# Optimization experiments

Hardware: AMD Instinct MI355X
Metric: run time of the kernel (lower is better)

Reference implementation:

```python
import jax, jax.numpy as jnp
import numpy as np

B, LQ, LK, C = 16, 1024, 1024, 512
WH = int(LQ ** 0.5)  # 32


def setup_inputs() -> dict:
    key = jax.random.key(0)
    ks = jax.random.split(key, 6)
    s1 = 1.0 / np.sqrt(LK)
    return {
        "query": jax.random.normal(ks[0], (B, LQ, C), jnp.float32),
        "key": jax.random.normal(ks[1], (B, LK, C), jnp.float32),
        "value": jax.random.normal(ks[2], (B, LK, C), jnp.float32),
        # nn.Linear weights, stored [out_features, in_features] like torch
        "w1": jax.random.normal(ks[3], (LK, LK), jnp.float32) * s1,
        "w2": jax.random.normal(ks[4], (LK, LK), jnp.float32) * s1,
        "w3": jax.random.normal(ks[5], (1, LK), jnp.float32) * s1,
    }


def reference(query, key, value, w1, w2, w3):
    # cosine-similarity matrix (computed under no_grad in the original)
    q = query / 100.0
    k = key / 100.0
    qn = jnp.sqrt(jnp.sum(q * q, axis=-1))[:, :, None]   # [B, LQ, 1]
    kn = jnp.sqrt(jnp.sum(k * k, axis=-1))[:, None, :]   # [B, 1, LK]
    outer = qn * kn                                       # rank-1 outer product [B, LQ, LK]
    upper = jnp.einsum('bqc,bkc->bqk', q, k)              # [B, LQ, LK]
    similar_rev = jax.lax.stop_gradient(upper / (outer + 1e-6))

    # 3-layer MLP gating over the LK axis -> scalar weight per query row
    h = jax.nn.gelu(jnp.einsum('bqk,ok->bqo', similar_rev, w1), approximate=False)
    h = jax.nn.gelu(jnp.einsum('bqk,ok->bqo', h, w2), approximate=False)
    w = jnp.einsum('bqk,ok->bqo', h, w3)[..., 0]          # [B, LQ]

    # weight^T @ similar_rev / wh, then tanh -> per-key scalar gate [B, LK, 1]
    weight = jnp.einsum('bq,bqk->bk', w, similar_rev) / WH
    weight = jnp.tanh(weight)[:, :, None]

    # value modulation + residual
    return value * weight + value
```

## Files before the change

### kernel.cpp

```cpp
#include <hip/hip_runtime.h>
#include <hip/hip_bf16.h>

#define B_  16
#define LQ_ 1024
#define LK_ 1024
#define C_  512

typedef __attribute__((ext_vector_type(4))) float f32x4;
typedef __attribute__((ext_vector_type(8))) short bf16x8;

__device__ __forceinline__ float bf2f(ushort u) {
  union { unsigned int i; float f; } v; v.i = ((unsigned int)u) << 16; return v.f;
}
__device__ __forceinline__ ushort f2bf(float f) {
  union { float f; unsigned int i; } v; v.f = f;
  unsigned int r = v.i + 0x7fffu + ((v.i >> 16) & 1u);
  return (ushort)(r >> 16);
}
__device__ __forceinline__ float gelu_exact(float x) {
  return 0.5f * x * (1.0f + erff(x * 0.70710678118654752f));
}

__device__ __forceinline__ void gload_lds16(const ushort* g, ushort* l) {
  __builtin_amdgcn_global_load_lds(
      (const __attribute__((address_space(1))) void*)g,
      (__attribute__((address_space(3))) void*)l, 16, 0, 0);
}

__global__ __launch_bounds__(256) void prep_qk(const float* __restrict__ x,
                                               ushort* __restrict__ xb,
                                               float* __restrict__ norms) {
  int wid = blockIdx.x * 4 + (threadIdx.x >> 6);
  int lane = threadIdx.x & 63;
  const float* xr = x + (long)wid * C_;
  ushort* xo = xb + (long)wid * C_;
  float ss = 0.f;
#pragma unroll
  for (int i0 = 0; i0 < 2; ++i0) {
    int i = lane * 4 + i0 * 256;
    float4 v = *(const float4*)(xr + i);
    ss += v.x * v.x + v.y * v.y + v.z * v.z + v.w * v.w;
    ushort4 o;
    o.x = f2bf(v.x); o.y = f2bf(v.y); o.z = f2bf(v.z); o.w = f2bf(v.w);
    *(ushort4*)(xo + i) = o;
  }
#pragma unroll
  for (int off = 32; off > 0; off >>= 1) ss += __shfl_xor(ss, off);
  if (lane == 0) norms[wid] = sqrtf(ss);
}

__global__ __launch_bounds__(256) void conv_bf16(const float* __restrict__ x,
                                                 ushort* __restrict__ o, int n4) {
  int i = blockIdx.x * 256 + threadIdx.x;
  if (i < n4) {
    float4 v = *(const float4*)(x + (long)i * 4);
    ushort4 u;
    u.x = f2bf(v.x); u.y = f2bf(v.y); u.z = f2bf(v.z); u.w = f2bf(v.w);
    *(ushort4*)(o + (long)i * 4) = u;
  }
}

#define BK 32

template <int EPI>
__global__ __launch_bounds__(256, 2) void gemm_nt(
    const ushort* __restrict__ A, const ushort* __restrict__ Bm,
    ushort* __restrict__ Cc, int K, long sA, long sB, long sC,
    const float* __restrict__ qn, const float* __restrict__ kn) {
  int b = blockIdx.z;
  A += (long)b * sA;
  Bm += (long)b * sB;
  Cc += (long)b * sC;
  const int bm = blockIdx.y * 128, bn = blockIdx.x * 128;

  __shared__ ushort At[128][32];
  __shared__ ushort Bt[128][32];

  int tid = threadIdx.x;
  int lane = tid & 63, w = tid >> 6;
  int wr = w >> 1, wc = w & 1;
  int l16 = lane & 15, lhi = lane >> 4;

  f32x4 acc[4][4] = {};

  int c0 = tid, c1 = tid + 256;
  int r0 = c0 >> 2, cb0 = (c0 & 3) ^ ((r0 >> 1) & 3);
  int r1 = c1 >> 2, cb1 = (c1 & 3) ^ ((r1 >> 1) & 3);
  int wbase0 = (tid & ~63);
  int wbase1 = wbase0 + 256;

  const ushort* Ar0 = A + (long)(bm + r0) * K + cb0 * 8;
  const ushort* Ar1 = A + (long)(bm + r1) * K + cb1 * 8;
  const ushort* Br0 = Bm + (long)(bn + r0) * K + cb0 * 8;
  const ushort* Br1 = Bm + (long)(bn + r1) * K + cb1 * 8;

  for (int k0 = 0; k0 < K; k0 += BK) {
    gload_lds16(Ar0 + k0, &At[0][0] + (size_t)wbase0 * 8);
    gload_lds16(Ar1 + k0, &At[0][0] + (size_t)wbase1 * 8);
    gload_lds16(Br0 + k0, &Bt[0][0] + (size_t)wbase0 * 8);
    gload_lds16(Br1 + k0, &Bt[0][0] + (size_t)wbase1 * 8);
    __syncthreads();

    bf16x8 af[4], bfr[4];
#pragma unroll
    for (int m = 0; m < 4; ++m) {
      int r = wr * 64 + m * 16 + l16;
      af[m] = *(const bf16x8*)&At[r][(lhi ^ ((r >> 1) & 3)) * 8];
    }
#pragma unroll
    for (int n = 0; n < 4; ++n) {
      int r = wc * 64 + n * 16 + l16;
      bfr[n] = *(const bf16x8*)&Bt[r][(lhi ^ ((r >> 1) & 3)) * 8];
    }
#pragma unroll
    for (int m = 0; m < 4; ++m)
#pragma unroll
      for (int n = 0; n < 4; ++n)
        acc[m][n] = __builtin_amdgcn_mfma_f32_16x16x32_bf16(af[m], bfr[n],
                                                            acc[m][n], 0, 0, 0);
    __syncthreads();
  }

#pragma unroll
  for (int m = 0; m < 4; ++m) {
    int row0 = bm + wr * 64 + m * 16 + lhi * 4;
#pragma unroll
    for (int n = 0; n < 4; ++n) {
      int col = bn + wc * 64 + n * 16 + l16;
#pragma unroll
      for (int r = 0; r < 4; ++r) {
        float v = acc[m][n][r];
        int grow = row0 + r;
        if (EPI == 0) {
          v = v / (qn[grow] * kn[col] + 1e-2f);
        } else {
          v = gelu_exact(v);
        }
        Cc[(long)grow * 1024 + col] = f2bf(v);
      }
    }
  }
}

__global__ __launch_bounds__(256) void wdot(const ushort* __restrict__ h2,
                                            const float* __restrict__ w3,
                                            float* __restrict__ wv) {
  int row = blockIdx.x * 4 + (threadIdx.x >> 6);
  int lane = threadIdx.x & 63;
  const ushort* hr = h2 + (long)row * LK_;
  float acc = 0.f;
#pragma unroll
  for (int i = 0; i < 2; ++i) {
    int idx = (lane + 64 * i) * 8;
    bf16x8 v = *(const bf16x8*)(hr + idx);
#pragma unroll
    for (int j = 0; j < 8; ++j) acc += bf2f((ushort)v[j]) * w3[idx + j];
  }
#pragma unroll
  for (int off = 32; off > 0; off >>= 1) acc += __shfl_xor(acc, off);
  if (lane == 0) wv[row] = acc;
}

__global__ __launch_bounds__(256) void gate_partial(const ushort* __restrict__ S,
                                                    const float* __restrict__ wv,
                                                    float* __restrict__ wraw) {
  int b = blockIdx.z;
  int k = blockIdx.x * 256 + threadIdx.x;
  int q0 = blockIdx.y * 128;
  const ushort* Sb = S + (long)b * LQ_ * LK_;
  const float* wb = wv + b * LQ_;
  float acc = 0.f;
#pragma unroll 4
  for (int q = q0; q < q0 + 128; ++q) acc += wb[q] * bf2f(Sb[(long)q * LK_ + k]);
  atomicAdd(&wraw[b * LK_ + k], acc);
}

__global__ __launch_bounds__(256) void finalize(const float* __restrict__ value,
                                                const float* __restrict__ wraw,
                                                float* __restrict__ out) {
  long i = (long)blockIdx.x * 256 + threadIdx.x;
  long e = i * 4;
  int row = (int)(e >> 9);
  float g = 1.f + tanhf(wraw[row] * (1.f / 32.f));
  float4 v = ((const float4*)value)[i];
  v.x *= g; v.y *= g; v.z *= g; v.w *= g;
  ((float4*)out)[i] = v;
}

extern "C" void kernel_launch(void* const* d_in, const int* in_sizes, int n_in,
                              void* d_out, int out_size, void* d_ws,
                              size_t ws_size, hipStream_t stream) {
  const float* query = (const float*)d_in[0];
  const float* key   = (const float*)d_in[1];
  const float* value = (const float*)d_in[2];
  const float* w1    = (const float*)d_in[3];
  const float* w2    = (const float*)d_in[4];
  const float* w3    = (const float*)d_in[5];
  float* out = (float*)d_out;

  const size_t QB_BYTES = (size_t)B_ * LQ_ * C_ * 2;
  const size_t S_BYTES  = (size_t)B_ * LQ_ * LK_ * 2;
  const size_t W_BYTES  = (size_t)LK_ * LK_ * 2;
  const size_t OFF_QB = 0;
  const size_t OFF_KB = OFF_QB + QB_BYTES;
  const size_t OFF_H2 = 0;
  const size_t OFF_S  = OFF_KB + QB_BYTES;
  const size_t OFF_H1 = OFF_S + S_BYTES;
  const size_t OFF_W1 = OFF_H1 + S_BYTES;
  const size_t OFF_W2 = OFF_W1 + W_BYTES;
  const size_t OFF_QN = OFF_W2 + W_BYTES;
  const size_t OFF_KN = OFF_QN + (size_t)B_ * LQ_ * 4;
  const size_t OFF_WV = OFF_KN + (size_t)B_ * LK_ * 4;
  const size_t OFF_WR = OFF_WV + (size_t)B_ * LQ_ * 4;
  const size_t TOTAL  = OFF_WR + (size_t)B_ * LK_ * 4;
  if (ws_size < TOTAL) return;

  char* ws = (char*)d_ws;
  ushort* Qb  = (ushort*)(ws + OFF_QB);
  ushort* Kb  = (ushort*)(ws + OFF_KB);
  ushort* S   = (ushort*)(ws + OFF_S);
  ushort* h1  = (ushort*)(ws + OFF_H1);
  ushort* h2  = (ushort*)(ws + OFF_H2);
  ushort* W1b = (ushort*)(ws + OFF_W1);
  ushort* W2b = (ushort*)(ws + OFF_W2);
  float* qn   = (float*)(ws + OFF_QN);
  float* kn   = (float*)(ws + OFF_KN);
  float* wv   = (float*)(ws + OFF_WV);
  float* wraw = (float*)(ws + OFF_WR);

  prep_qk<<<dim3(B_ * LQ_ / 4), 256, 0, stream>>>(query, Qb, qn);
  prep_qk<<<dim3(B_ * LK_ / 4), 256, 0, stream>>>(key, Kb, kn);
  conv_bf16<<<dim3(LK_ * LK_ / 4 / 256), 256, 0, stream>>>(w1, W1b, LK_ * LK_ / 4);
  conv_bf16<<<dim3(LK_ * LK_ / 4 / 256), 256, 0, stream>>>(w2, W2b, LK_ * LK_ / 4);
  hipMemsetAsync(wraw, 0, (size_t)B_ * LK_ * 4, stream);

  gemm_nt<0><<<dim3(8, 8, B_), 256, 0, stream>>>(
      Qb, Kb, S, C_, (long)LQ_ * C_, (long)LK_ * C_, (long)LQ_ * LK_, qn, kn);

  gemm_nt<1><<<dim3(8, 8, B_), 256, 0, stream>>>(
      S, W1b, h1, LK_, (long)LQ_ * LK_, 0L, (long)LQ_ * LK_, nullptr, nullptr);

  gemm_nt<1><<<dim3(8, 8, B_), 256, 0, stream>>>(
      h1, W2b, h2, LK_, (long)LQ_ * LK_, 0L, (long)LQ_ * LK_, nullptr, nullptr);

  wdot<<<dim3(B_ * LQ_ / 4), 256, 0, stream>>>(h2, w3, wv);

  gate_partial<<<dim3(LK_ / 256, LQ_ / 128, B_), 256, 0, stream>>>(S, wv, wraw);

  finalize<<<dim3((size_t)B_ * LK_ * C_ / 4 / 256), 256, 0, stream>>>(value, wraw, out);
}
```

Baseline: 199.7 us.

## Double-buffer GEMM LDS tiles and remap blocks for XCD-local batch grouping

Turns the GEMM main loop into a two-stage pipeline: the next K-tile is loaded into a second LDS buffer while the current one feeds the MFMAs, which drops one barrier per iteration. The 3D grid becomes a flat 1D grid whose block index is permuted as (orig&7)*per + (orig>>3). This places contiguous tiles of the same batch on the same XCD, so A and B tiles get more L2 reuse. The cost is double the LDS footprint (32KB per block), which could limit how many blocks fit per CU.

```diff
diff --git a/kernel.cpp b/kernel.cpp
--- a/kernel.cpp
+++ b/kernel.cpp
@@ -67,14 +67,19 @@
     const ushort* __restrict__ A, const ushort* __restrict__ Bm,
     ushort* __restrict__ Cc, int K, long sA, long sB, long sC,
     const float* __restrict__ qn, const float* __restrict__ kn) {
-  int b = blockIdx.z;
+  int per = (int)(gridDim.x >> 3);
+  int orig = blockIdx.x;
+  int id = (orig & 7) * per + (orig >> 3);
+  int b = id >> 6;
+  int rtile = id & 63;
+  const int bm = (rtile >> 3) * 128, bn = (rtile & 7) * 128;
+
   A += (long)b * sA;
   Bm += (long)b * sB;
   Cc += (long)b * sC;
-  const int bm = blockIdx.y * 128, bn = blockIdx.x * 128;
-
-  __shared__ ushort At[128][32];
-  __shared__ ushort Bt[128][32];
+
+  __shared__ ushort At[2][128][32];
+  __shared__ ushort Bt[2][128][32];
 
   int tid = threadIdx.x;
   int lane = tid & 63, w = tid >> 6;
@@ -94,23 +99,39 @@
   const ushort* Br0 = Bm + (long)(bn + r0) * K + cb0 * 8;
   const ushort* Br1 = Bm + (long)(bn + r1) * K + cb1 * 8;
 
-  for (int k0 = 0; k0 < K; k0 += BK) {
-    gload_lds16(Ar0 + k0, &At[0][0] + (size_t)wbase0 * 8);
-    gload_lds16(Ar1 + k0, &At[0][0] + (size_t)wbase1 * 8);
-    gload_lds16(Br0 + k0, &Bt[0][0] + (size_t)wbase0 * 8);
-    gload_lds16(Br1 + k0, &Bt[0][0] + (size_t)wbase1 * 8);
-    __syncthreads();
+  const int nt = K / BK;
+  {
+    ushort* Ad = &At[0][0][0];
+    ushort* Bd = &Bt[0][0][0];
+    gload_lds16(Ar0, Ad + (size_t)wbase0 * 8);
+    gload_lds16(Ar1, Ad + (size_t)wbase1 * 8);
+    gload_lds16(Br0, Bd + (size_t)wbase0 * 8);
+    gload_lds16(Br1, Bd + (size_t)wbase1 * 8);
+  }
+  __syncthreads();
+
+  int cur = 0;
+  for (int t = 0; t < nt; ++t) {
+    if (t + 1 < nt) {
+      int k1 = (t + 1) * BK;
+      ushort* Ad = &At[cur ^ 1][0][0];
+      ushort* Bd = &Bt[cur ^ 1][0][0];
+      gload_lds16(Ar0 + k1, Ad + (size_t)wbase0 * 8);
+      gload_lds16(Ar1 + k1, Ad + (size_t)wbase1 * 8);
+      gload_lds16(Br0 + k1, Bd + (size_t)wbase0 * 8);
+      gload_lds16(Br1 + k1, Bd + (size_t)wbase1 * 8);
+    }
 
     bf16x8 af[4], bfr[4];
 #pragma unroll
     for (int m = 0; m < 4; ++m) {
       int r = wr * 64 + m * 16 + l16;
-      af[m] = *(const bf16x8*)&At[r][(lhi ^ ((r >> 1) & 3)) * 8];
+      af[m] = *(const bf16x8*)&At[cur][r][(lhi ^ ((r >> 1) & 3)) * 8];
     }
 #pragma unroll
     for (int n = 0; n < 4; ++n) {
       int r = wc * 64 + n * 16 + l16;
-      bfr[n] = *(const bf16x8*)&Bt[r][(lhi ^ ((r >> 1) & 3)) * 8];
+      bfr[n] = *(const bf16x8*)&Bt[cur][r][(lhi ^ ((r >> 1) & 3)) * 8];
     }
 #pragma unroll
     for (int m = 0; m < 4; ++m)
@@ -119,6 +140,7 @@
         acc[m][n] = __builtin_amdgcn_mfma_f32_16x16x32_bf16(af[m], bfr[n],
                                                             acc[m][n], 0, 0, 0);
     __syncthreads();
+    cur ^= 1;
   }
 
 #pragma unroll
@@ -234,13 +256,13 @@
   conv_bf16<<<dim3(LK_ * LK_ / 4 / 256), 256, 0, stream>>>(w2, W2b, LK_ * LK_ / 4);
   hipMemsetAsync(wraw, 0, (size_t)B_ * LK_ * 4, stream);
 
-  gemm_nt<0><<<dim3(8, 8, B_), 256, 0, stream>>>(
+  gemm_nt<0><<<dim3(1024), 256, 0, stream>>>(
       Qb, Kb, S, C_, (long)LQ_ * C_, (long)LK_ * C_, (long)LQ_ * LK_, qn, kn);
 
-  gemm_nt<1><<<dim3(8, 8, B_), 256, 0, stream>>>(
+  gemm_nt<1><<<dim3(1024), 256, 0, stream>>>(
       S, W1b, h1, LK_, (long)LQ_ * LK_, 0L, (long)LQ_ * LK_, nullptr, nullptr);
 
-  gemm_nt<1><<<dim3(8, 8, B_), 256, 0, stream>>>(
+  gemm_nt<1><<<dim3(1024), 256, 0, stream>>>(
       h1, W2b, h2, LK_, (long)LQ_ * LK_, 0L, (long)LQ_ * LK_, nullptr, nullptr);
 
   wdot<<<dim3(B_ * LQ_ / 4), 256, 0, stream>>>(h2, w3, wv);
```

New measurement: 177.6 us. 11.1% less time.
